# Performance work log

Measured on AMD Instinct MI355X. Metric: run time of the kernel, lower is better.

## Reference

```python
import jax, jax.numpy as jnp
import numpy as np

T, D, H = 8192, 128, 1024  # seq_len, obs_dim, lstm_hidden_size


def setup_inputs() -> dict:
    key = jax.random.key(0)
    ks = jax.random.split(key, 9)
    lim = 1.0 / np.sqrt(H)  # eqx LSTMCell/Linear uniform init scale

    def u(k, shape):
        return jax.random.uniform(k, shape, minval=-lim, maxval=lim, dtype=jnp.float32)

    obs = jax.random.normal(ks[0], (T, D), dtype=jnp.float32)
    W_ih0 = u(ks[1], (4 * H, D))
    W_hh0 = u(ks[2], (4 * H, H))
    b0 = u(ks[3], (4 * H,))
    W_ih1 = u(ks[4], (4 * H, H))
    W_hh1 = u(ks[5], (4 * H, H))
    b1 = u(ks[6], (4 * H,))
    W_dec = u(ks[7], (2 * D, H))
    b_dec = u(ks[8], (2 * D,))
    return {"obs": obs, "W_ih0": W_ih0, "W_hh0": W_hh0, "b0": b0,
            "W_ih1": W_ih1, "W_hh1": W_hh1, "b1": b1,
            "W_dec": W_dec, "b_dec": b_dec}


def _lstm_cell(gx, h, c, W_hh):
    # gx: (4H,) precomputed input projection + bias; h, c: (H,)
    z = gx + W_hh @ h
    i, f, g, o = jnp.split(z, 4)
    i = jax.nn.sigmoid(i)
    f = jax.nn.sigmoid(f)
    g = jnp.tanh(g)
    o = jax.nn.sigmoid(o)
    c_new = f * c + i * g
    h_new = o * jnp.tanh(c_new)
    return h_new, c_new


def reference(obs, W_ih0, W_hh0, b0, W_ih1, W_hh1, b1, W_dec, b_dec):
    d = obs.shape[1]
    hdim = W_hh0.shape[1]
    # teacher forcing: input at step t is obs[t-1], obs[-1] replaced by zeros
    shifted = jnp.concatenate([jnp.zeros((1, d), obs.dtype), obs[:-1]], axis=0)
    # layer-0 input projection is input-only -> precompute as one big GEMM (T, 4H)
    gx0_all = shifted @ W_ih0.T + b0

    def step(state, gx0_t):
        (h0, c0), (h1, c1) = state
        h0, c0 = _lstm_cell(gx0_t, h0, c0, W_hh0)
        gx1 = W_ih1 @ h0 + b1
        h1, c1 = _lstm_cell(gx1, h1, c1, W_hh1)
        return ((h0, c0), (h1, c1)), h1

    z = jnp.zeros((hdim,), obs.dtype)
    init = ((z, z), (z, z))
    _, all_h = jax.lax.scan(step, init, gx0_all)  # all_h: (T, H)

    params = all_h @ W_dec.T + b_dec  # (T, 2D)
    loc = params[:, :d]
    scale = jax.nn.softplus(params[:, d:]) + 1e-4
    return loc, scale
```

## Files before the change

### kernel.cpp

```cpp
#include <hip/hip_runtime.h>
#include <math.h>

#define TT 8192
#define DD 128
#define HH 1024
#define RINGN 64
#define NA 64
#define NB 128
#define NC 16
#define NWG (NA + NB + NC)


typedef unsigned long long ull;

__device__ __forceinline__ ull ldpair(const ull* p) {
  return __hip_atomic_load(p, __ATOMIC_RELAXED, __HIP_MEMORY_SCOPE_AGENT);
}
__device__ __forceinline__ void stpair(ull* p, float v, unsigned e) {
  ull u = ((ull)e << 32) | (ull)__float_as_uint(v);
  __hip_atomic_store(p, u, __ATOMIC_RELAXED, __HIP_MEMORY_SCOPE_AGENT);
}
__device__ __forceinline__ unsigned ldflag(const unsigned* p) {
  return __hip_atomic_load(p, __ATOMIC_RELAXED, __HIP_MEMORY_SCOPE_AGENT);
}
__device__ __forceinline__ void stflag(unsigned* p, unsigned v) {
  __hip_atomic_store(p, v, __ATOMIC_RELAXED, __HIP_MEMORY_SCOPE_AGENT);
}
__device__ __forceinline__ float sigm(float x) { return 1.0f / (1.0f + expf(-x)); }
__device__ __forceinline__ float softplusf(float x) {
  return x > 0.0f ? x + log1pf(expf(-x)) : log1pf(expf(x));
}

#define FMA16(W)                                                      \
  a0 = fmaf(W[0][4*i+0], h4.x, a0); a0 = fmaf(W[0][4*i+1], h4.y, a0); \
  a0 = fmaf(W[0][4*i+2], h4.z, a0); a0 = fmaf(W[0][4*i+3], h4.w, a0); \
  a1 = fmaf(W[1][4*i+0], h4.x, a1); a1 = fmaf(W[1][4*i+1], h4.y, a1); \
  a1 = fmaf(W[1][4*i+2], h4.z, a1); a1 = fmaf(W[1][4*i+3], h4.w, a1); \
  a2 = fmaf(W[2][4*i+0], h4.x, a2); a2 = fmaf(W[2][4*i+1], h4.y, a2); \
  a2 = fmaf(W[2][4*i+2], h4.z, a2); a2 = fmaf(W[2][4*i+3], h4.w, a2); \
  a3 = fmaf(W[3][4*i+0], h4.x, a3); a3 = fmaf(W[3][4*i+1], h4.y, a3); \
  a3 = fmaf(W[3][4*i+2], h4.z, a3); a3 = fmaf(W[3][4*i+3], h4.w, a3);

__global__ void __launch_bounds__(512, 1) deepar_persistent(
    const float* __restrict__ obs,
    const float* __restrict__ Wih0, const float* __restrict__ Whh0, const float* __restrict__ b0,
    const float* __restrict__ Wih1, const float* __restrict__ Whh1, const float* __restrict__ b1,
    const float* __restrict__ Wdec, const float* __restrict__ bdec,
    float* __restrict__ out,
    unsigned* b_cons, unsigned* c_cons,
    unsigned* a_fA, unsigned* a_fB, unsigned* b_fB, unsigned* b_fC,
    ull* h0A, ull* h0B, ull* h1B, ull* h1C)
{
  __shared__ __align__(16) float hx[2][2304];

  const int wg   = blockIdx.x;
  const int tid  = threadIdx.x;
  const int wid  = tid >> 6;
  const int lane = tid & 63;

  if (wg < NA) {
    const int rg = tid >> 5;
    const int q  = tid & 31;
    const int j  = wg * 16 + rg;
    const int k0 = q * 36;
    float w[4][36];
    #pragma unroll
    for (int i = 0; i < 9; ++i) {
      const int kb = k0 + 4 * i;
      #pragma unroll
      for (int r = 0; r < 4; ++r) {
        const float* src = (kb < HH) ? (Whh0 + (size_t)(r * HH + j) * HH + kb)
                                     : (Wih0 + (size_t)(r * HH + j) * DD + (kb - HH));
        const float4 v = *(const float4*)src;
        w[r][4*i+0] = v.x; w[r][4*i+1] = v.y; w[r][4*i+2] = v.z; w[r][4*i+3] = v.w;
      }
    }
    float bs[4];
    #pragma unroll
    for (int r = 0; r < 4; ++r) bs[r] = b0[r * HH + j];
    float creg = 0.0f;

    for (int t = 0; t < TT; ++t) {
      float a0 = 0.f, a1 = 0.f, a2 = 0.f, a3 = 0.f;
      if (t > 0) {
        const float* obr = obs + (size_t)(t - 1) * DD;
        #pragma unroll
        for (int i = 0; i < 9; ++i) {
          const int kb = k0 + 4 * i;
          if (kb >= HH) { const float4 h4 = *(const float4*)(obr + (kb - HH)); FMA16(w) }
        }
      }
      if (wid == 1 && ((t & 15) == 0) && t >= 48) {
        const unsigned need = (unsigned)(t - 32);
        while (!__all((ldflag(&b_cons[lane]) >= need) &
                      (ldflag(&b_cons[lane + 64]) >= need))) {}
      }
      if (wid == 0 && t > 0) {
        const unsigned tg = (unsigned)t;
        while (!__all((lane == wg) | (ldflag(&a_fA[lane]) >= tg))) {}
      }
      __builtin_amdgcn_s_barrier();
      float* Lb = hx[t & 1];
      if (t > 0) {
        const ull* sl = h0A + (size_t)((t - 1) & (RINGN - 1)) * HH;
        const unsigned ee = (unsigned)t;
        ull u0 = ldpair(sl + tid);
        ull u1 = ldpair(sl + tid + 512);
        while ((unsigned)(u0 >> 32) != ee) u0 = ldpair(sl + tid);
        Lb[tid] = __uint_as_float((unsigned)u0);
        while ((unsigned)(u1 >> 32) != ee) u1 = ldpair(sl + tid + 512);
        Lb[tid + 512] = __uint_as_float((unsigned)u1);
      }
      __syncthreads();
      if (t > 0) {
        #pragma unroll
        for (int i = 0; i < 9; ++i) {
          const int kb = k0 + 4 * i;
          if (kb < HH) { const float4 h4 = *(const float4*)&Lb[kb]; FMA16(w) }
        }
      }
      #pragma unroll
      for (int s = 1; s < 32; s <<= 1) {
        a0 += __shfl_xor(a0, s); a1 += __shfl_xor(a1, s);
        a2 += __shfl_xor(a2, s); a3 += __shfl_xor(a3, s);
      }
      if (q == 0) {
        const float ig = sigm(a0 + bs[0]);
        const float fg = sigm(a1 + bs[1]);
        const float gg = tanhf(a2 + bs[2]);
        const float og = sigm(a3 + bs[3]);
        creg = fg * creg + ig * gg;
        const float hv = og * tanhf(creg);
        const size_t off = (size_t)(t & (RINGN - 1)) * HH + j;
        const unsigned ep = (unsigned)(t + 1);
        stpair(&h0A[off], hv, ep);
        stpair(&h0B[off], hv, ep);
      }
      asm volatile("" ::: "memory");
      __builtin_amdgcn_s_barrier();
      if (tid == 0) { stflag(&a_fA[wg], (unsigned)(t + 1));
                      stflag(&a_fB[wg], (unsigned)(t + 1)); }
    }

  } else if (wg < NA + NB) {
    const int rg = tid >> 6;
    const int q  = tid & 63;
    const int s_ = wg - NA;
    const int j  = s_ * 8 + rg;
    const int k0 = q * 32;
    float w[4][32];
    #pragma unroll
    for (int i = 0; i < 8; ++i) {
      const int kb = k0 + 4 * i;
      #pragma unroll
      for (int r = 0; r < 4; ++r) {
        const float* src = (kb < HH) ? (Wih1 + (size_t)(r * HH + j) * HH + kb)
                                     : (Whh1 + (size_t)(r * HH + j) * HH + (kb - HH));
        const float4 v = *(const float4*)src;
        w[r][4*i+0] = v.x; w[r][4*i+1] = v.y; w[r][4*i+2] = v.z; w[r][4*i+3] = v.w;
      }
    }
    float bs[4];
    #pragma unroll
    for (int r = 0; r < 4; ++r) bs[r] = b1[r * HH + j];
    float creg = 0.0f;
    const int p0 = tid + 4 * (tid >> 5);
    const int p1 = p0 + 576;
    const int p2 = p0 + 1152;
    const int p3 = p2 + 576;
    const int baseB = (q < 32) ? q * 36 : 1152 + (q - 32) * 36;

    for (int t = 0; t < TT; ++t) {
      if (wid == 2 && ((t & 15) == 0) && t >= 48) {
        const unsigned need = (unsigned)(t - 32);
        while (!__all((lane >= NC) | (ldflag(&c_cons[lane]) >= need))) {}
      }
      if (wid == 0) {
        const unsigned eA = (unsigned)(t + 1);
        const unsigned eB = (unsigned)t;
        for (;;) {
          int ok = (ldflag(&a_fB[lane]) >= eA);
          if (t > 0) {
            ok &= (lane == s_)        | (ldflag(&b_fB[lane])      >= eB);
            ok &= ((lane + 64) == s_) | (ldflag(&b_fB[lane + 64]) >= eB);
          }
          if (__all(ok)) break;
        }
      }
      __builtin_amdgcn_s_barrier();
      float* Lb = hx[t & 1];
      {
        const ull* s0 = h0B + (size_t)(t & (RINGN - 1)) * HH;
        const ull* s1 = h1B + (size_t)((t - 1) & (RINGN - 1)) * HH;
        const unsigned e0 = (unsigned)(t + 1);
        const unsigned e1 = (unsigned)t;
        ull u0 = ldpair(s0 + tid);
        ull u1 = ldpair(s0 + tid + 512);
        ull u2 = ldpair(s1 + tid);
        ull u3 = ldpair(s1 + tid + 512);
        while ((unsigned)(u0 >> 32) != e0) u0 = ldpair(s0 + tid);
        Lb[p0] = __uint_as_float((unsigned)u0);
        while ((unsigned)(u1 >> 32) != e0) u1 = ldpair(s0 + tid + 512);
        Lb[p1] = __uint_as_float((unsigned)u1);
        while ((unsigned)(u2 >> 32) != e1) u2 = ldpair(s1 + tid);
        Lb[p2] = __uint_as_float((unsigned)u2);
        while ((unsigned)(u3 >> 32) != e1) u3 = ldpair(s1 + tid + 512);
        Lb[p3] = __uint_as_float((unsigned)u3);
      }
      __syncthreads();
      if (tid == 0) stflag(&b_cons[s_], (unsigned)(t + 1));
      float a0 = 0.f, a1 = 0.f, a2 = 0.f, a3 = 0.f;
      #pragma unroll
      for (int i = 0; i < 8; ++i) {
        const float4 h4 = *(const float4*)&Lb[baseB + 4 * i];
        FMA16(w)
      }
      #pragma unroll
      for (int s = 1; s < 64; s <<= 1) {
        a0 += __shfl_xor(a0, s); a1 += __shfl_xor(a1, s);
        a2 += __shfl_xor(a2, s); a3 += __shfl_xor(a3, s);
      }
      if (q == 0) {
        const float ig = sigm(a0 + bs[0]);
        const float fg = sigm(a1 + bs[1]);
        const float gg = tanhf(a2 + bs[2]);
        const float og = sigm(a3 + bs[3]);
        creg = fg * creg + ig * gg;
        const float hv = og * tanhf(creg);
        const size_t off = (size_t)(t & (RINGN - 1)) * HH + j;
        const unsigned ep = (unsigned)(t + 1);
        stpair(&h1B[off], hv, ep);
        stpair(&h1C[off], hv, ep);
      }
      asm volatile("" ::: "memory");
      __builtin_amdgcn_s_barrier();
      if (tid == 0) { stflag(&b_fB[s_], (unsigned)(t + 1));
                      stflag(&b_fC[s_], (unsigned)(t + 1)); }
    }

  } else {
    const int rg = tid >> 6;
    const int q  = tid & 63;
    const int cg = wg - NA - NB;
    const int row0 = cg * 16 + 2 * rg;
    const int k0 = q * 16;
    float w[2][16];
    #pragma unroll
    for (int i = 0; i < 4; ++i) {
      const int kb = k0 + 4 * i;
      #pragma unroll
      for (int r = 0; r < 2; ++r) {
        const float4 v = *(const float4*)(Wdec + (size_t)(row0 + r) * HH + kb);
        w[r][4*i+0] = v.x; w[r][4*i+1] = v.y; w[r][4*i+2] = v.z; w[r][4*i+3] = v.w;
      }
    }
    const float bs0 = bdec[row0], bs1 = bdec[row0 + 1];
    const int pc0 = tid + 4 * (tid >> 4);
    const int pc1 = pc0 + 640;

    for (int t = 0; t < TT; ++t) {
      if (wid == 0) {
        const unsigned tg = (unsigned)(t + 1);
        while (!__all((ldflag(&b_fC[lane]) >= tg) &
                      (ldflag(&b_fC[lane + 64]) >= tg))) {}
      }
      __builtin_amdgcn_s_barrier();
      float* Lb = hx[t & 1];
      {
        const ull* sl = h1C + (size_t)(t & (RINGN - 1)) * HH;
        const unsigned ee = (unsigned)(t + 1);
        ull u0 = ldpair(sl + tid);
        ull u1 = ldpair(sl + tid + 512);
        while ((unsigned)(u0 >> 32) != ee) u0 = ldpair(sl + tid);
        Lb[pc0] = __uint_as_float((unsigned)u0);
        while ((unsigned)(u1 >> 32) != ee) u1 = ldpair(sl + tid + 512);
        Lb[pc1] = __uint_as_float((unsigned)u1);
      }
      __syncthreads();
      if (tid == 0) stflag(&c_cons[cg], (unsigned)(t + 1));
      float a0 = 0.f, a1 = 0.f;
      {
        const int base = q * 20;
        #pragma unroll
        for (int i = 0; i < 4; ++i) {
          const float4 h4 = *(const float4*)&Lb[base + 4 * i];
          a0 = fmaf(w[0][4*i+0], h4.x, a0); a0 = fmaf(w[0][4*i+1], h4.y, a0);
          a0 = fmaf(w[0][4*i+2], h4.z, a0); a0 = fmaf(w[0][4*i+3], h4.w, a0);
          a1 = fmaf(w[1][4*i+0], h4.x, a1); a1 = fmaf(w[1][4*i+1], h4.y, a1);
          a1 = fmaf(w[1][4*i+2], h4.z, a1); a1 = fmaf(w[1][4*i+3], h4.w, a1);
        }
      }
      #pragma unroll
      for (int s = 1; s < 64; s <<= 1) { a0 += __shfl_xor(a0, s); a1 += __shfl_xor(a1, s); }
      if (q == 0) {
        const float z0 = a0 + bs0;
        const float z1 = a1 + bs1;
        if (row0 < DD) {
          out[(size_t)t * DD + row0]     = z0;
          out[(size_t)t * DD + row0 + 1] = z1;
        } else {
          out[(size_t)TT * DD + (size_t)t * DD + (row0 - DD)]     = softplusf(z0) + 1e-4f;
          out[(size_t)TT * DD + (size_t)t * DD + (row0 - DD) + 1] = softplusf(z1) + 1e-4f;
        }
      }
    }
  }
}

extern "C" void kernel_launch(void* const* d_in, const int* in_sizes, int n_in,
                              void* d_out, int out_size, void* d_ws, size_t ws_size,
                              hipStream_t stream) {
  const float* obs  = (const float*)d_in[0];
  const float* Wih0 = (const float*)d_in[1];
  const float* Whh0 = (const float*)d_in[2];
  const float* b0   = (const float*)d_in[3];
  const float* Wih1 = (const float*)d_in[4];
  const float* Whh1 = (const float*)d_in[5];
  const float* b1   = (const float*)d_in[6];
  const float* Wdec = (const float*)d_in[7];
  const float* bdec = (const float*)d_in[8];
  float* out = (float*)d_out;

  const size_t RB = (size_t)RINGN * HH * 8;
  unsigned char* ws = (unsigned char*)d_ws;
  unsigned* b_cons = (unsigned*)(ws);
  unsigned* c_cons = (unsigned*)(ws + 512);
  unsigned* a_fA   = (unsigned*)(ws + 1024);
  unsigned* a_fB   = (unsigned*)(ws + 1536);
  unsigned* b_fB   = (unsigned*)(ws + 2048);
  unsigned* b_fC   = (unsigned*)(ws + 2560);
  ull* h0A = (ull*)(ws + 4096);
  ull* h0B = (ull*)(ws + 4096 + RB);
  ull* h1B = (ull*)(ws + 4096 + 2 * RB);
  ull* h1C = (ull*)(ws + 4096 + 3 * RB);

  hipMemsetAsync(ws, 0, 4096 + 4 * RB, stream);

  hipLaunchKernelGGL(deepar_persistent, dim3(NWG), dim3(512), 0, stream,
                     obs, Wih0, Whh0, b0, Wih1, Whh1, b1, Wdec, bdec, out,
                     b_cons, c_cons, a_fA, a_fB, b_fB, b_fC,
                     h0A, h0B, h1B, h1C);
}
```

Before: 31.53 ms.

## Fold decoder into layer-1 workgroups, drop separate decoder group and h1C ring

Removes the 16 dedicated decoder workgroups and their h1C ring, consumer flags and back-pressure polling. Each layer-1 workgroup now has waves 2 and 3 compute one decoder row for step t-1, reusing the h1 values it already stages into LDS for its own recurrence. The loop runs one extra iteration to finish the last decoder step. It also adds an s_waitcnt vmcnt(0) drain before the barrier that precedes flag publication. The intent is to shorten the chain of global handoffs and reduce polling traffic, at the cost of extra per-step work on the layer-1 critical path.

Result: slower. 34.40 ms, median of 3 (+9.1%).

```diff
diff --git a/kernel.cpp b/kernel.cpp
--- a/kernel.cpp
+++ b/kernel.cpp
@@ -7,8 +7,7 @@
 #define RINGN 64
 #define NA 64
 #define NB 128
-#define NC 16
-#define NWG (NA + NB + NC)
+#define NWG (NA + NB)
 
 
 typedef unsigned long long ull;
@@ -30,6 +29,9 @@
 __device__ __forceinline__ float softplusf(float x) {
   return x > 0.0f ? x + log1pf(expf(-x)) : log1pf(expf(x));
 }
+
+#define DRAIN()  asm volatile("s_waitcnt vmcnt(0)" ::: "memory")
+#define CFENCE() asm volatile("" ::: "memory")
 
 #define FMA16(W)                                                      \
   a0 = fmaf(W[0][4*i+0], h4.x, a0); a0 = fmaf(W[0][4*i+1], h4.y, a0); \
@@ -47,9 +49,8 @@
     const float* __restrict__ Wih1, const float* __restrict__ Whh1, const float* __restrict__ b1,
     const float* __restrict__ Wdec, const float* __restrict__ bdec,
     float* __restrict__ out,
-    unsigned* b_cons, unsigned* c_cons,
-    unsigned* a_fA, unsigned* a_fB, unsigned* b_fB, unsigned* b_fC,
-    ull* h0A, ull* h0B, ull* h1B, ull* h1C)
+    unsigned* b_cons, unsigned* a_fA, unsigned* a_fB, unsigned* b_fB,
+    ull* h0A, ull* h0B, ull* h1B)
 {
   __shared__ __align__(16) float hx[2][2304];
 
@@ -136,13 +137,14 @@
         stpair(&h0A[off], hv, ep);
         stpair(&h0B[off], hv, ep);
       }
-      asm volatile("" ::: "memory");
+      DRAIN();
       __builtin_amdgcn_s_barrier();
+      CFENCE();
       if (tid == 0) { stflag(&a_fA[wg], (unsigned)(t + 1));
                       stflag(&a_fB[wg], (unsigned)(t + 1)); }
     }
 
-  } else if (wg < NA + NB) {
+  } else {
     const int rg = tid >> 6;
     const int q  = tid & 63;
     const int s_ = wg - NA;
@@ -169,17 +171,26 @@
     const int p2 = p0 + 1152;
     const int p3 = p2 + 576;
     const int baseB = (q < 32) ? q * 36 : 1152 + (q - 32) * 36;
-
-    for (int t = 0; t < TT; ++t) {
-      if (wid == 2 && ((t & 15) == 0) && t >= 48) {
-        const unsigned need = (unsigned)(t - 32);
-        while (!__all((lane >= NC) | (ldflag(&c_cons[lane]) >= need))) {}
-      }
+    const int crow = s_ * 2 + (wid - 2);
+    float wd[16];
+    float bsd = 0.0f;
+    if (wid == 2 || wid == 3) {
+      #pragma unroll
+      for (int i = 0; i < 4; ++i) {
+        const float4 v = *(const float4*)(Wdec + (size_t)crow * HH + lane * 16 + 4 * i);
+        wd[4*i+0] = v.x; wd[4*i+1] = v.y; wd[4*i+2] = v.z; wd[4*i+3] = v.w;
+      }
+      bsd = bdec[crow];
+    }
+    const int dbase = 1152 + lane * 16 + 4 * ((lane * 16) >> 5);
+
+    for (int t = 0; t <= TT; ++t) {
       if (wid == 0) {
         const unsigned eA = (unsigned)(t + 1);
         const unsigned eB = (unsigned)t;
         for (;;) {
-          int ok = (ldflag(&a_fB[lane]) >= eA);
+          int ok = 1;
+          if (t < TT) ok &= (ldflag(&a_fB[lane]) >= eA);
           if (t > 0) {
             ok &= (lane == s_)        | (ldflag(&b_fB[lane])      >= eB);
             ok &= ((lane + 64) == s_) | (ldflag(&b_fB[lane + 64]) >= eB);
@@ -190,117 +201,68 @@
       __builtin_amdgcn_s_barrier();
       float* Lb = hx[t & 1];
       {
-        const ull* s0 = h0B + (size_t)(t & (RINGN - 1)) * HH;
-        const ull* s1 = h1B + (size_t)((t - 1) & (RINGN - 1)) * HH;
         const unsigned e0 = (unsigned)(t + 1);
         const unsigned e1 = (unsigned)t;
-        ull u0 = ldpair(s0 + tid);
-        ull u1 = ldpair(s0 + tid + 512);
+        if (t < TT) {
+          const ull* s0 = h0B + (size_t)(t & (RINGN - 1)) * HH;
+          ull u0 = ldpair(s0 + tid);
+          ull u1 = ldpair(s0 + tid + 512);
+          while ((unsigned)(u0 >> 32) != e0) u0 = ldpair(s0 + tid);
+          Lb[p0] = __uint_as_float((unsigned)u0);
+          while ((unsigned)(u1 >> 32) != e0) u1 = ldpair(s0 + tid + 512);
+          Lb[p1] = __uint_as_float((unsigned)u1);
+        }
+        const ull* s1 = h1B + (size_t)((t - 1) & (RINGN - 1)) * HH;
         ull u2 = ldpair(s1 + tid);
         ull u3 = ldpair(s1 + tid + 512);
-        while ((unsigned)(u0 >> 32) != e0) u0 = ldpair(s0 + tid);
-        Lb[p0] = __uint_as_float((unsigned)u0);
-        while ((unsigned)(u1 >> 32) != e0) u1 = ldpair(s0 + tid + 512);
-        Lb[p1] = __uint_as_float((unsigned)u1);
         while ((unsigned)(u2 >> 32) != e1) u2 = ldpair(s1 + tid);
         Lb[p2] = __uint_as_float((unsigned)u2);
         while ((unsigned)(u3 >> 32) != e1) u3 = ldpair(s1 + tid + 512);
         Lb[p3] = __uint_as_float((unsigned)u3);
       }
       __syncthreads();
-      if (tid == 0) stflag(&b_cons[s_], (unsigned)(t + 1));
-      float a0 = 0.f, a1 = 0.f, a2 = 0.f, a3 = 0.f;
-      #pragma unroll
-      for (int i = 0; i < 8; ++i) {
-        const float4 h4 = *(const float4*)&Lb[baseB + 4 * i];
-        FMA16(w)
-      }
-      #pragma unroll
-      for (int s = 1; s < 64; s <<= 1) {
-        a0 += __shfl_xor(a0, s); a1 += __shfl_xor(a1, s);
-        a2 += __shfl_xor(a2, s); a3 += __shfl_xor(a3, s);
-      }
-      if (q == 0) {
-        const float ig = sigm(a0 + bs[0]);
-        const float fg = sigm(a1 + bs[1]);
-        const float gg = tanhf(a2 + bs[2]);
-        const float og = sigm(a3 + bs[3]);
-        creg = fg * creg + ig * gg;
-        const float hv = og * tanhf(creg);
-        const size_t off = (size_t)(t & (RINGN - 1)) * HH + j;
-        const unsigned ep = (unsigned)(t + 1);
-        stpair(&h1B[off], hv, ep);
-        stpair(&h1C[off], hv, ep);
-      }
-      asm volatile("" ::: "memory");
-      __builtin_amdgcn_s_barrier();
-      if (tid == 0) { stflag(&b_fB[s_], (unsigned)(t + 1));
-                      stflag(&b_fC[s_], (unsigned)(t + 1)); }
-    }
-
-  } else {
-    const int rg = tid >> 6;
-    const int q  = tid & 63;
-    const int cg = wg - NA - NB;
-    const int row0 = cg * 16 + 2 * rg;
-    const int k0 = q * 16;
-    float w[2][16];
-    #pragma unroll
-    for (int i = 0; i < 4; ++i) {
-      const int kb = k0 + 4 * i;
-      #pragma unroll
-      for (int r = 0; r < 2; ++r) {
-        const float4 v = *(const float4*)(Wdec + (size_t)(row0 + r) * HH + kb);
-        w[r][4*i+0] = v.x; w[r][4*i+1] = v.y; w[r][4*i+2] = v.z; w[r][4*i+3] = v.w;
-      }
-    }
-    const float bs0 = bdec[row0], bs1 = bdec[row0 + 1];
-    const int pc0 = tid + 4 * (tid >> 4);
-    const int pc1 = pc0 + 640;
-
-    for (int t = 0; t < TT; ++t) {
-      if (wid == 0) {
-        const unsigned tg = (unsigned)(t + 1);
-        while (!__all((ldflag(&b_fC[lane]) >= tg) &
-                      (ldflag(&b_fC[lane + 64]) >= tg))) {}
-      }
-      __builtin_amdgcn_s_barrier();
-      float* Lb = hx[t & 1];
-      {
-        const ull* sl = h1C + (size_t)(t & (RINGN - 1)) * HH;
-        const unsigned ee = (unsigned)(t + 1);
-        ull u0 = ldpair(sl + tid);
-        ull u1 = ldpair(sl + tid + 512);
-        while ((unsigned)(u0 >> 32) != ee) u0 = ldpair(sl + tid);
-        Lb[pc0] = __uint_as_float((unsigned)u0);
-        while ((unsigned)(u1 >> 32) != ee) u1 = ldpair(sl + tid + 512);
-        Lb[pc1] = __uint_as_float((unsigned)u1);
-      }
-      __syncthreads();
-      if (tid == 0) stflag(&c_cons[cg], (unsigned)(t + 1));
-      float a0 = 0.f, a1 = 0.f;
-      {
-        const int base = q * 20;
+      if (tid == 64 && t < TT) stflag(&b_cons[s_], (unsigned)(t + 1));
+      if (t < TT) {
+        float a0 = 0.f, a1 = 0.f, a2 = 0.f, a3 = 0.f;
+        #pragma unroll
+        for (int i = 0; i < 8; ++i) {
+          const float4 h4 = *(const float4*)&Lb[baseB + 4 * i];
+          FMA16(w)
+        }
+        #pragma unroll
+        for (int s = 1; s < 64; s <<= 1) {
+          a0 += __shfl_xor(a0, s); a1 += __shfl_xor(a1, s);
+          a2 += __shfl_xor(a2, s); a3 += __shfl_xor(a3, s);
+        }
+        if (q == 0) {
+          const float ig = sigm(a0 + bs[0]);
+          const float fg = sigm(a1 + bs[1]);
+          const float gg = tanhf(a2 + bs[2]);
+          const float og = sigm(a3 + bs[3]);
+          creg = fg * creg + ig * gg;
+          stpair(&h1B[(size_t)(t & (RINGN - 1)) * HH + j], og * tanhf(creg),
+                 (unsigned)(t + 1));
+        }
+        DRAIN();
+        __builtin_amdgcn_s_barrier();
+        CFENCE();
+        if (tid == 0) stflag(&b_fB[s_], (unsigned)(t + 1));
+      }
+      if (t > 0 && (wid == 2 || wid == 3)) {
+        float a = 0.f;
         #pragma unroll
         for (int i = 0; i < 4; ++i) {
-          const float4 h4 = *(const float4*)&Lb[base + 4 * i];
-          a0 = fmaf(w[0][4*i+0], h4.x, a0); a0 = fmaf(w[0][4*i+1], h4.y, a0);
-          a0 = fmaf(w[0][4*i+2], h4.z, a0); a0 = fmaf(w[0][4*i+3], h4.w, a0);
-          a1 = fmaf(w[1][4*i+0], h4.x, a1); a1 = fmaf(w[1][4*i+1], h4.y, a1);
-          a1 = fmaf(w[1][4*i+2], h4.z, a1); a1 = fmaf(w[1][4*i+3], h4.w, a1);
-        }
-      }
-      #pragma unroll
-      for (int s = 1; s < 64; s <<= 1) { a0 += __shfl_xor(a0, s); a1 += __shfl_xor(a1, s); }
-      if (q == 0) {
-        const float z0 = a0 + bs0;
-        const float z1 = a1 + bs1;
-        if (row0 < DD) {
-          out[(size_t)t * DD + row0]     = z0;
-          out[(size_t)t * DD + row0 + 1] = z1;
-        } else {
-          out[(size_t)TT * DD + (size_t)t * DD + (row0 - DD)]     = softplusf(z0) + 1e-4f;
-          out[(size_t)TT * DD + (size_t)t * DD + (row0 - DD) + 1] = softplusf(z1) + 1e-4f;
+          const float4 h4 = *(const float4*)&Lb[dbase + 4 * i];
+          a = fmaf(wd[4*i+0], h4.x, a); a = fmaf(wd[4*i+1], h4.y, a);
+          a = fmaf(wd[4*i+2], h4.z, a); a = fmaf(wd[4*i+3], h4.w, a);
+        }
+        #pragma unroll
+        for (int s = 1; s < 64; s <<= 1) a += __shfl_xor(a, s);
+        if (lane == 0) {
+          const float z = a + bsd;
+          if (crow < DD) out[(size_t)(t - 1) * DD + crow] = z;
+          else out[(size_t)TT * DD + (size_t)(t - 1) * DD + (crow - DD)]
+                 = softplusf(z) + 1e-4f;
         }
       }
     }
@@ -324,20 +286,16 @@
   const size_t RB = (size_t)RINGN * HH * 8;
   unsigned char* ws = (unsigned char*)d_ws;
   unsigned* b_cons = (unsigned*)(ws);
-  unsigned* c_cons = (unsigned*)(ws + 512);
   unsigned* a_fA   = (unsigned*)(ws + 1024);
   unsigned* a_fB   = (unsigned*)(ws + 1536);
   unsigned* b_fB   = (unsigned*)(ws + 2048);
-  unsigned* b_fC   = (unsigned*)(ws + 2560);
   ull* h0A = (ull*)(ws + 4096);
   ull* h0B = (ull*)(ws + 4096 + RB);
   ull* h1B = (ull*)(ws + 4096 + 2 * RB);
-  ull* h1C = (ull*)(ws + 4096 + 3 * RB);
-
-  hipMemsetAsync(ws, 0, 4096 + 4 * RB, stream);
+
+  hipMemsetAsync(ws, 0, 4096 + 3 * RB, stream);
 
   hipLaunchKernelGGL(deepar_persistent, dim3(NWG), dim3(512), 0, stream,
                      obs, Wih0, Whh0, b0, Wih1, Whh1, b1, Wdec, bdec, out,
-                     b_cons, c_cons, a_fA, a_fB, b_fB, b_fC,
-                     h0A, h0B, h1B, h1C);
-}
+                     b_cons, a_fA, a_fB, b_fB, h0A, h0B, h1B);
+}
```
